# Kernel tuning notes

Measured on AMD Instinct MI355X. Metric: run time of the kernel, lower is better.

Reference implementation:

```python
import jax, jax.numpy as jnp
import numpy as np

N_DRUGS, N_TARGETS, N_ENT = 2000, 4000, 6000
NUM_RELS, REL_DIM, FEAT = 8, 64, 512
N_TRI = 131072
IN1 = 2 * FEAT + REL_DIM  # 1088


def setup_inputs() -> dict:
    key = jax.random.key(0)
    ks = jax.random.split(key, 12)
    # id2rel pattern: utype = drug iff r % 2 == 0; vtype = drug iff (r // 2) % 2 == 0
    rels = np.arange(NUM_RELS)
    u_is_drug = jnp.asarray(rels % 2 == 0)
    v_is_drug = jnp.asarray((rels // 2) % 2 == 0)
    triplets = jnp.stack([
        jax.random.randint(ks[0], (N_TRI,), 0, N_ENT, dtype=jnp.int32),
        jax.random.randint(ks[1], (N_TRI,), 0, N_ENT, dtype=jnp.int32),
        jax.random.randint(ks[2], (N_TRI,), 0, NUM_RELS, dtype=jnp.int32),
    ], axis=1)
    return {
        "d_intra": jax.random.normal(ks[3], (N_DRUGS, FEAT), jnp.float32),
        "d_inter": jax.random.normal(ks[4], (N_DRUGS, FEAT), jnp.float32),
        "t_intra": jax.random.normal(ks[5], (N_TARGETS, FEAT), jnp.float32),
        "t_inter": jax.random.normal(ks[6], (N_TARGETS, FEAT), jnp.float32),
        "did_sub": jax.random.randint(ks[7], (N_ENT,), 0, N_DRUGS, dtype=jnp.int32),
        "tid_sub": jax.random.randint(ks[8], (N_ENT,), 0, N_TARGETS, dtype=jnp.int32),
        "triplets": triplets,
        "u_is_drug": u_is_drug,
        "v_is_drug": v_is_drug,
        "rel_emb_intra": jax.random.normal(ks[9], (NUM_RELS, REL_DIM), jnp.float32) * 0.1,
        "rel_emb_inter": jax.random.normal(ks[10], (NUM_RELS, REL_DIM), jnp.float32) * 0.1,
        "W_intra": jax.random.normal(ks[11], (IN1, 1), jnp.float32) * 0.03,
        "b_intra": jnp.zeros((1,), jnp.float32),
        "W_inter": jax.random.normal(jax.random.fold_in(key, 99), (IN1, 1), jnp.float32) * 0.03,
        "b_inter": jnp.zeros((1,), jnp.float32),
    }


def _branch_logits(d_feat, t_feat, rel_emb, W, b, did, tid, u, v, r, u_drug, v_drug):
    # Conditional gather: drug-table row if type is 'drug', else target-table row.
    fu = jnp.where(u_drug[:, None], d_feat[did[u]], t_feat[tid[u]])  # [N, FEAT]
    fv = jnp.where(v_drug[:, None], d_feat[did[v]], t_feat[tid[v]])  # [N, FEAT]
    re = rel_emb[r]                                                  # [N, REL_DIM]
    # Equivalent to concat([fu, fv, re]) @ W + b, done blockwise (no big concat).
    Wu, Wv, Wr = W[:FEAT], W[FEAT:2 * FEAT], W[2 * FEAT:]
    return fu @ Wu + fv @ Wv + re @ Wr + b  # [N, 1]


def reference(d_intra, d_inter, t_intra, t_inter, did_sub, tid_sub, triplets,
              u_is_drug, v_is_drug, rel_emb_intra, rel_emb_inter,
              W_intra, b_intra, W_inter, b_inter):
    a1, a2 = 0.6, 0.2
    u, v, r = triplets[:, 0], triplets[:, 1], triplets[:, 2]
    ud, vd = u_is_drug[r], v_is_drug[r]  # per-triplet type flags via id2rel[r]
    s1 = _branch_logits(d_intra, t_intra, rel_emb_intra, W_intra, b_intra,
                        did_sub, tid_sub, u, v, r, ud, vd)
    s2 = _branch_logits(d_inter, t_inter, rel_emb_inter, W_inter, b_inter,
                        did_sub, tid_sub, u, v, r, ud, vd)
    return a1 * jnp.tanh(s1) + a2 * jnp.tanh(s2)
```

## Files before the change

kernel.cpp:

```cpp
#include <hip/hip_runtime.h>

#define FEAT 512
#define REL_DIM 64
#define N_DRUGS 2000
#define N_TARGETS 4000
#define N_TRI 131072

__device__ __forceinline__ float dot4(float4 a, float4 b) {
    return a.x * b.x + a.y * b.y + a.z * b.z + a.w * b.w;
}

__device__ __forceinline__ float waveReduce(float v) {
#pragma unroll
    for (int off = 32; off; off >>= 1) v += __shfl_xor(v, off, 64);
    return v;
}

__global__ __launch_bounds__(256) void precompute_kernel(
    const float* __restrict__ d_intra, const float* __restrict__ d_inter,
    const float* __restrict__ t_intra, const float* __restrict__ t_inter,
    const float* __restrict__ rel_emb_intra, const float* __restrict__ rel_emb_inter,
    const float* __restrict__ W_intra, const float* __restrict__ b_intra,
    const float* __restrict__ W_inter, const float* __restrict__ b_inter,
    float* __restrict__ preD, float* __restrict__ preT,
    float* __restrict__ rel1, float* __restrict__ rel2)
{
    const int wave = threadIdx.x >> 6;
    const int lane = threadIdx.x & 63;
    const int row  = blockIdx.x * 4 + wave;

    if (row < N_DRUGS + N_TARGETS) {
        const float* fA;
        const float* fB;
        float* outp;
        if (row < N_DRUGS) {
            fA = d_intra + (size_t)row * FEAT;
            fB = d_inter + (size_t)row * FEAT;
            outp = preD + row * 4;
        } else {
            const int t = row - N_DRUGS;
            fA = t_intra + (size_t)t * FEAT;
            fB = t_inter + (size_t)t * FEAT;
            outp = preT + t * 4;
        }
        const float4* a4 = (const float4*)fA;
        const float4* b4 = (const float4*)fB;
        const float4* w1 = (const float4*)W_intra;
        const float4* w2 = (const float4*)W_inter;

        const float4 aA0 = a4[lane],        aA1 = a4[lane + 64];
        const float4 bB0 = b4[lane],        bB1 = b4[lane + 64];
        const float4 wu10 = w1[lane],       wu11 = w1[lane + 64];
        const float4 wv10 = w1[lane + 128], wv11 = w1[lane + 192];
        const float4 wu20 = w2[lane],       wu21 = w2[lane + 64];
        const float4 wv20 = w2[lane + 128], wv21 = w2[lane + 192];

        float s_u1 = dot4(aA0, wu10) + dot4(aA1, wu11);
        float s_v1 = dot4(aA0, wv10) + dot4(aA1, wv11);
        float s_u2 = dot4(bB0, wu20) + dot4(bB1, wu21);
        float s_v2 = dot4(bB0, wv20) + dot4(bB1, wv21);

        s_u1 = waveReduce(s_u1);
        s_v1 = waveReduce(s_v1);
        s_u2 = waveReduce(s_u2);
        s_v2 = waveReduce(s_v2);

        if (lane == 0) {
            outp[0] = s_u1;
            outp[1] = s_v1;
            outp[2] = s_u2;
            outp[3] = s_v2;
        }
    } else if (row == N_DRUGS + N_TARGETS) {
        const float b1 = b_intra[0];
        const float b2 = b_inter[0];
        const float wr1 = W_intra[2 * FEAT + lane];
        const float wr2 = W_inter[2 * FEAT + lane];
#pragma unroll
        for (int r = 0; r < 8; ++r) {
            float p1 = rel_emb_intra[r * REL_DIM + lane] * wr1;
            float p2 = rel_emb_inter[r * REL_DIM + lane] * wr2;
            p1 = waveReduce(p1);
            p2 = waveReduce(p2);
            if (lane == 0) {
                rel1[r] = p1 + b1;
                rel2[r] = p2 + b2;
            }
        }
    }
}

__global__ __launch_bounds__(256) void triplet_kernel(
    const int* __restrict__ triplets,
    const int* __restrict__ did_sub, const int* __restrict__ tid_sub,
    const float* __restrict__ preD, const float* __restrict__ preT,
    const float* __restrict__ rel1, const float* __restrict__ rel2,
    float* __restrict__ out)
{
    const int i = blockIdx.x * blockDim.x + threadIdx.x;
    if (i >= N_TRI) return;

    const int u = triplets[3 * i + 0];
    const int v = triplets[3 * i + 1];
    const int r = triplets[3 * i + 2];

    const bool ud = (r & 1) == 0;
    const bool vd = ((r >> 1) & 1) == 0;

    float cu1, cu2, cv1, cv2;
    if (ud) { const int d = did_sub[u]; cu1 = preD[d * 4 + 0]; cu2 = preD[d * 4 + 2]; }
    else    { const int t = tid_sub[u]; cu1 = preT[t * 4 + 0]; cu2 = preT[t * 4 + 2]; }
    if (vd) { const int d = did_sub[v]; cv1 = preD[d * 4 + 1]; cv2 = preD[d * 4 + 3]; }
    else    { const int t = tid_sub[v]; cv1 = preT[t * 4 + 1]; cv2 = preT[t * 4 + 3]; }

    const float s1 = cu1 + cv1 + rel1[r];
    const float s2 = cu2 + cv2 + rel2[r];
    out[i] = 0.6f * tanhf(s1) + 0.2f * tanhf(s2);
}

extern "C" void kernel_launch(void* const* d_in, const int* in_sizes, int n_in,
                              void* d_out, int out_size, void* d_ws, size_t ws_size,
                              hipStream_t stream) {
    const float* d_intra        = (const float*)d_in[0];
    const float* d_inter        = (const float*)d_in[1];
    const float* t_intra        = (const float*)d_in[2];
    const float* t_inter        = (const float*)d_in[3];
    const int*   did_sub        = (const int*)d_in[4];
    const int*   tid_sub        = (const int*)d_in[5];
    const int*   triplets       = (const int*)d_in[6];
    const float* rel_emb_intra  = (const float*)d_in[9];
    const float* rel_emb_inter  = (const float*)d_in[10];
    const float* W_intra        = (const float*)d_in[11];
    const float* b_intra        = (const float*)d_in[12];
    const float* W_inter        = (const float*)d_in[13];
    const float* b_inter        = (const float*)d_in[14];

    float* ws   = (float*)d_ws;
    float* preD = ws;
    float* preT = ws + N_DRUGS * 4;
    float* rel1 = preT + N_TARGETS * 4;
    float* rel2 = rel1 + 8;

    const int rows = N_DRUGS + N_TARGETS + 1;
    const int gridA = (rows + 3) / 4;
    precompute_kernel<<<gridA, 256, 0, stream>>>(
        d_intra, d_inter, t_intra, t_inter,
        rel_emb_intra, rel_emb_inter,
        W_intra, b_intra, W_inter, b_inter,
        preD, preT, rel1, rel2);

    const int gridB = (N_TRI + 255) / 256;
    triplet_kernel<<<gridB, 256, 0, stream>>>(
        triplets, did_sub, tid_sub, preD, preT, rel1, rel2, (float*)d_out);
}
```

Baseline: 101.0 us.

## Process two triplets per thread with packed float2 tables and fast tanh

Each thread in the triplet kernel now handles two triplets, reading them as three int2 loads and writing a float2 result. The precomputed per-entity scalars are repacked into unified float2 U and V tables, and the two relation constants are merged into one float2 table, so each lookup is a single 8-byte load. Both did_sub and tid_sub are loaded unconditionally to avoid divergent branches, and tanhf is replaced by an exp-plus-reciprocal approximation. The gains come from fewer load instructions and less divergence, at the cost of extra index loads and slightly lower tanh accuracy.

```diff
diff --git a/kernel.cpp b/kernel.cpp
--- a/kernel.cpp
+++ b/kernel.cpp
@@ -4,6 +4,7 @@
 #define REL_DIM 64
 #define N_DRUGS 2000
 #define N_TARGETS 4000
+#define N_ENT_ROWS (N_DRUGS + N_TARGETS)
 #define N_TRI 131072
 
 __device__ __forceinline__ float dot4(float4 a, float4 b) {
@@ -16,32 +17,34 @@
     return v;
 }
 
+__device__ __forceinline__ float fast_tanh(float x) {
+    const float e = __expf(2.0f * x);
+    return 1.0f - 2.0f * __builtin_amdgcn_rcpf(e + 1.0f);
+}
+
 __global__ __launch_bounds__(256) void precompute_kernel(
     const float* __restrict__ d_intra, const float* __restrict__ d_inter,
     const float* __restrict__ t_intra, const float* __restrict__ t_inter,
     const float* __restrict__ rel_emb_intra, const float* __restrict__ rel_emb_inter,
     const float* __restrict__ W_intra, const float* __restrict__ b_intra,
     const float* __restrict__ W_inter, const float* __restrict__ b_inter,
-    float* __restrict__ preD, float* __restrict__ preT,
-    float* __restrict__ rel1, float* __restrict__ rel2)
+    float2* __restrict__ preU, float2* __restrict__ preV,
+    float2* __restrict__ relC)
 {
     const int wave = threadIdx.x >> 6;
     const int lane = threadIdx.x & 63;
     const int row  = blockIdx.x * 4 + wave;
 
-    if (row < N_DRUGS + N_TARGETS) {
+    if (row < N_ENT_ROWS) {
         const float* fA;
         const float* fB;
-        float* outp;
         if (row < N_DRUGS) {
             fA = d_intra + (size_t)row * FEAT;
             fB = d_inter + (size_t)row * FEAT;
-            outp = preD + row * 4;
         } else {
             const int t = row - N_DRUGS;
             fA = t_intra + (size_t)t * FEAT;
             fB = t_inter + (size_t)t * FEAT;
-            outp = preT + t * 4;
         }
         const float4* a4 = (const float4*)fA;
         const float4* b4 = (const float4*)fB;
@@ -66,12 +69,10 @@
         s_v2 = waveReduce(s_v2);
 
         if (lane == 0) {
-            outp[0] = s_u1;
-            outp[1] = s_v1;
-            outp[2] = s_u2;
-            outp[3] = s_v2;
+            preU[row] = make_float2(s_u1, s_u2);
+            preV[row] = make_float2(s_v1, s_v2);
         }
-    } else if (row == N_DRUGS + N_TARGETS) {
+    } else if (row == N_ENT_ROWS) {
         const float b1 = b_intra[0];
         const float b2 = b_inter[0];
         const float wr1 = W_intra[2 * FEAT + lane];
@@ -82,40 +83,45 @@
             float p2 = rel_emb_inter[r * REL_DIM + lane] * wr2;
             p1 = waveReduce(p1);
             p2 = waveReduce(p2);
-            if (lane == 0) {
-                rel1[r] = p1 + b1;
-                rel2[r] = p2 + b2;
-            }
+            if (lane == 0) relC[r] = make_float2(p1 + b1, p2 + b2);
         }
     }
 }
 
 __global__ __launch_bounds__(256) void triplet_kernel(
-    const int* __restrict__ triplets,
+    const int2* __restrict__ tri2,
     const int* __restrict__ did_sub, const int* __restrict__ tid_sub,
-    const float* __restrict__ preD, const float* __restrict__ preT,
-    const float* __restrict__ rel1, const float* __restrict__ rel2,
-    float* __restrict__ out)
+    const float2* __restrict__ preU, const float2* __restrict__ preV,
+    const float2* __restrict__ relC,
+    float2* __restrict__ out2)
 {
     const int i = blockIdx.x * blockDim.x + threadIdx.x;
-    if (i >= N_TRI) return;
+    const int2 p0 = tri2[3 * i + 0];
+    const int2 p1 = tri2[3 * i + 1];
+    const int2 p2 = tri2[3 * i + 2];
 
-    const int u = triplets[3 * i + 0];
-    const int v = triplets[3 * i + 1];
-    const int r = triplets[3 * i + 2];
+    const int us[2] = {p0.x, p1.y};
+    const int vs[2] = {p0.y, p2.x};
+    const int rs[2] = {p1.x, p2.y};
+    float res[2];
 
-    const bool ud = (r & 1) == 0;
-    const bool vd = ((r >> 1) & 1) == 0;
-
-    float cu1, cu2, cv1, cv2;
-    if (ud) { const int d = did_sub[u]; cu1 = preD[d * 4 + 0]; cu2 = preD[d * 4 + 2]; }
-    else    { const int t = tid_sub[u]; cu1 = preT[t * 4 + 0]; cu2 = preT[t * 4 + 2]; }
-    if (vd) { const int d = did_sub[v]; cv1 = preD[d * 4 + 1]; cv2 = preD[d * 4 + 3]; }
-    else    { const int t = tid_sub[v]; cv1 = preT[t * 4 + 1]; cv2 = preT[t * 4 + 3]; }
-
-    const float s1 = cu1 + cv1 + rel1[r];
-    const float s2 = cu2 + cv2 + rel2[r];
-    out[i] = 0.6f * tanhf(s1) + 0.2f * tanhf(s2);
+#pragma unroll
+    for (int k = 0; k < 2; ++k) {
+        const int u = us[k], v = vs[k], r = rs[k];
+        const bool ud = (r & 1) == 0;
+        const bool vd = ((r >> 1) & 1) == 0;
+        const int du = did_sub[u], tu = tid_sub[u];
+        const int dv = did_sub[v], tv = tid_sub[v];
+        const int iu = ud ? du : tu + N_DRUGS;
+        const int iv = vd ? dv : tv + N_DRUGS;
+        const float2 cu = preU[iu];
+        const float2 cv = preV[iv];
+        const float2 cr = relC[r];
+        const float s1 = cu.x + cv.x + cr.x;
+        const float s2 = cu.y + cv.y + cr.y;
+        res[k] = 0.6f * fast_tanh(s1) + 0.2f * fast_tanh(s2);
+    }
+    out2[i] = make_float2(res[0], res[1]);
 }
 
 extern "C" void kernel_launch(void* const* d_in, const int* in_sizes, int n_in,
@@ -135,21 +141,20 @@
     const float* W_inter        = (const float*)d_in[13];
     const float* b_inter        = (const float*)d_in[14];
 
-    float* ws   = (float*)d_ws;
-    float* preD = ws;
-    float* preT = ws + N_DRUGS * 4;
-    float* rel1 = preT + N_TARGETS * 4;
-    float* rel2 = rel1 + 8;
+    float2* ws   = (float2*)d_ws;
+    float2* preU = ws;
+    float2* preV = ws + N_ENT_ROWS;
+    float2* relC = preV + N_ENT_ROWS;
 
-    const int rows = N_DRUGS + N_TARGETS + 1;
+    const int rows  = N_ENT_ROWS + 1;
     const int gridA = (rows + 3) / 4;
     precompute_kernel<<<gridA, 256, 0, stream>>>(
         d_intra, d_inter, t_intra, t_inter,
         rel_emb_intra, rel_emb_inter,
         W_intra, b_intra, W_inter, b_inter,
-        preD, preT, rel1, rel2);
+        preU, preV, relC);
 
-    const int gridB = (N_TRI + 255) / 256;
+    const int gridB = (N_TRI / 2 + 255) / 256;
     triplet_kernel<<<gridB, 256, 0, stream>>>(
-        triplets, did_sub, tid_sub, preD, preT, rel1, rel2, (float*)d_out);
+        (const int2*)triplets, did_sub, tid_sub, preU, preV, relC, (float2*)d_out);
 }
```

Result: no change. 101.9 us, median of 2 (+0.9%).
